# Kernel optimization log

Hardware: AMD Instinct MI355X
Metric: run time of the kernel (lower is better)

The kernel has to match this reference:

```python
import jax, jax.numpy as jnp
import numpy as np

B, H, W, D, K = 32, 64, 64, 128, 1024

def setup_inputs() -> dict:
    key = jax.random.key(0)
    k1, k2 = jax.random.split(key)
    inputs = jax.random.normal(k1, (B, H, W, D), dtype=jnp.float32)
    embedding = jax.random.normal(k2, (D, K), dtype=jnp.float32)  # codebook, column per code
    return {"inputs": inputs, "embedding": embedding}

def reference(inputs, embedding):
    D_ = embedding.shape[0]
    x = inputs.reshape(-1, D_)                                  # [N, D]
    dist = (jnp.sum(x * x, axis=-1, keepdims=True)
            - 2.0 * (x @ embedding)
            + jnp.sum(embedding * embedding, axis=0, keepdims=True))  # [N, K]
    idx = jnp.argmax(-dist, axis=1).reshape(inputs.shape[:-1])  # [B, H, W]
    return embedding.T[idx]                                     # [B, H, W, D]
```

## Files before the change

### kernel.cpp

```cpp
#include <hip/hip_runtime.h>

#define KC 1024
#define DD 128
#define NT_COUNT (KC / 16)
#define RPB 64

typedef short bf16x8 __attribute__((ext_vector_type(8)));
typedef float f32x4  __attribute__((ext_vector_type(4)));

#define AS1 __attribute__((address_space(1)))
#define AS3 __attribute__((address_space(3)))

static __device__ __forceinline__ unsigned short f2bf(float f) {
    unsigned u = __float_as_uint(f);
    unsigned r = (u + 0x7fffu + ((u >> 16) & 1u)) >> 16;
    return (unsigned short)r;
}
static __device__ __forceinline__ float bf2f(unsigned short h) {
    return __uint_as_float(((unsigned)h) << 16);
}
static __device__ __forceinline__ void gl_lds16(const void* g, void* l) {
    __builtin_amdgcn_global_load_lds((const AS1 void*)g, (AS3 void*)l, 16, 0, 0);
}
static __device__ __forceinline__ void gl_lds4(const void* g, void* l) {
    __builtin_amdgcn_global_load_lds((const AS1 void*)g, (AS3 void*)l, 4, 0, 0);
}

__global__ __launch_bounds__(256) void vq_prep(const float* __restrict__ E,
                                               float* __restrict__ e2h,
                                               float* __restrict__ ET,
                                               unsigned short* __restrict__ Bpk) {
    __shared__ float T[16 * 129];
    const int nt  = blockIdx.x;
    const int tid = threadIdx.x;

    for (int i = tid; i < 16 * DD; i += 256) {
        int d  = i >> 4;
        int kk = i & 15;
        T[kk * 129 + d] = E[(size_t)d * KC + nt * 16 + kk];
    }
    __syncthreads();

    if (tid < 16) {
        float s = 0.f;
#pragma unroll 16
        for (int d = 0; d < DD; ++d) {
            float v = T[tid * 129 + d];
            s = fmaf(v, v, s);
        }
        e2h[nt * 16 + tid] = 512.0f - 0.5f * s;
    }

    for (int i = tid; i < 16 * DD; i += 256) {
        int kk = i >> 7;
        int d  = i & 127;
        ET[(size_t)(nt * 16 + kk) * DD + d] = T[kk * 129 + d];
    }

    {
        const int s    = tid >> 6;
        const int lane = tid & 63;
        const int kk   = lane & 15;
        const int d0   = s * 32 + (lane >> 4) * 8;
        bf16x8 hi, lo;
#pragma unroll
        for (int j = 0; j < 8; ++j) {
            float v = T[kk * 129 + d0 + j];
            unsigned short h = f2bf(v);
            hi[j] = (short)h;
            lo[j] = (short)f2bf(v - bf2f(h));
        }
        char* base = (char*)Bpk + (size_t)nt * 8192 + s * 1024 + lane * 16;
        *(bf16x8*)(base)        = hi;
        *(bf16x8*)(base + 4096) = lo;
    }
}

__global__ __launch_bounds__(64, 2) void vq_main(const float* __restrict__ X,
                                                 const float* __restrict__ e2h,
                                                 const float* __restrict__ ET,
                                                 const unsigned short* __restrict__ Bpk,
                                                 float* __restrict__ Out) {
    __shared__ __align__(16) char lds[2 * 8448];
    int*   s_k1  = (int*)(lds);
    int*   s_k2  = (int*)(lds + 256);
    int*   s_win = (int*)(lds + 512);
    float* s_gap = (float*)(lds + 768);

    const int lane  = threadIdx.x;
    const int quad  = lane >> 4;
    const int n16   = lane & 15;
    const int wrow0 = blockIdx.x * RPB;
    const int lidx16 = lane * 16;
    const int lidx4  = lane * 4;

    bf16x8 ahi[4][4], alo[4][4];
#pragma unroll
    for (int t = 0; t < 4; ++t) {
#pragma unroll
        for (int s = 0; s < 4; ++s) {
            const int row = wrow0 + t * 16 + n16;
            const int d0  = s * 32 + quad * 8;
            const float4 p = *(const float4*)(X + (size_t)row * DD + d0);
            const float4 q = *(const float4*)(X + (size_t)row * DD + d0 + 4);
            float v[8] = {p.x, p.y, p.z, p.w, q.x, q.y, q.z, q.w};
#pragma unroll
            for (int j = 0; j < 8; ++j) {
                unsigned short h = f2bf(v[j]);
                ahi[t][s][j] = (short)h;
                alo[t][s][j] = (short)f2bf(v[j] - bf2f(h));
            }
        }
    }

    float p1[4][4], p2[4][4];
#pragma unroll
    for (int t = 0; t < 4; ++t)
#pragma unroll
        for (int r = 0; r < 4; ++r) { p1[t][r] = 0.0f; p2[t][r] = 0.0f; }

#define STAGE(NT, BOFF)                                                          \
    do {                                                                         \
        const char* g = (const char*)Bpk + (size_t)(NT) * 8192;                  \
        _Pragma("unroll")                                                        \
        for (int c = 0; c < 8; ++c)                                              \
            gl_lds16(g + c * 1024 + lidx16, lds + (BOFF) + c * 1024);            \
        gl_lds4(e2h + (NT) * 16 + n16, lds + (BOFF) + 8192);                     \
    } while (0)

#define TILE(NT, BOFF)                                                           \
    do {                                                                         \
        const char* l = lds + (BOFF);                                            \
        const bf16x8 bh0 = *(const bf16x8*)(l + 0 * 1024 + lidx16);              \
        const bf16x8 bh1 = *(const bf16x8*)(l + 1 * 1024 + lidx16);              \
        const bf16x8 bh2 = *(const bf16x8*)(l + 2 * 1024 + lidx16);              \
        const bf16x8 bh3 = *(const bf16x8*)(l + 3 * 1024 + lidx16);              \
        const bf16x8 bl0 = *(const bf16x8*)(l + 4 * 1024 + lidx16);              \
        const bf16x8 bl1 = *(const bf16x8*)(l + 5 * 1024 + lidx16);              \
        const bf16x8 bl2 = *(const bf16x8*)(l + 6 * 1024 + lidx16);              \
        const bf16x8 bl3 = *(const bf16x8*)(l + 7 * 1024 + lidx16);              \
        const float  ev  = *(const float*)(l + 8192 + lidx4);                    \
        const unsigned ntinv = (unsigned)(63 - (NT));                            \
        _Pragma("unroll")                                                        \
        for (int t = 0; t < 4; ++t) {                                            \
            f32x4 acc = {ev, ev, ev, ev};                                        \
            acc = __builtin_amdgcn_mfma_f32_16x16x32_bf16(ahi[t][0], bh0, acc, 0, 0, 0); \
            acc = __builtin_amdgcn_mfma_f32_16x16x32_bf16(ahi[t][1], bh1, acc, 0, 0, 0); \
            acc = __builtin_amdgcn_mfma_f32_16x16x32_bf16(ahi[t][2], bh2, acc, 0, 0, 0); \
            acc = __builtin_amdgcn_mfma_f32_16x16x32_bf16(ahi[t][3], bh3, acc, 0, 0, 0); \
            acc = __builtin_amdgcn_mfma_f32_16x16x32_bf16(alo[t][0], bh0, acc, 0, 0, 0); \
            acc = __builtin_amdgcn_mfma_f32_16x16x32_bf16(alo[t][1], bh1, acc, 0, 0, 0); \
            acc = __builtin_amdgcn_mfma_f32_16x16x32_bf16(alo[t][2], bh2, acc, 0, 0, 0); \
            acc = __builtin_amdgcn_mfma_f32_16x16x32_bf16(alo[t][3], bh3, acc, 0, 0, 0); \
            acc = __builtin_amdgcn_mfma_f32_16x16x32_bf16(ahi[t][0], bl0, acc, 0, 0, 0); \
            acc = __builtin_amdgcn_mfma_f32_16x16x32_bf16(ahi[t][1], bl1, acc, 0, 0, 0); \
            acc = __builtin_amdgcn_mfma_f32_16x16x32_bf16(ahi[t][2], bl2, acc, 0, 0, 0); \
            acc = __builtin_amdgcn_mfma_f32_16x16x32_bf16(ahi[t][3], bl3, acc, 0, 0, 0); \
            _Pragma("unroll")                                                    \
            for (int r = 0; r < 4; ++r) {                                        \
                float v = __uint_as_float((__float_as_uint(acc[r]) & ~63u) | ntinv); \
                float lo = fminf(p1[t][r], v);                                   \
                p1[t][r] = fmaxf(p1[t][r], v);                                   \
                p2[t][r] = fmaxf(p2[t][r], lo);                                  \
            }                                                                    \
        }                                                                        \
    } while (0)

    STAGE(0, 0);
    for (int nt = 0; nt < NT_COUNT; nt += 2) {
        STAGE(nt + 1, 8448);
        __builtin_amdgcn_s_waitcnt(3961);
        __builtin_amdgcn_sched_barrier(0);
        TILE(nt, 0);
        if (nt + 2 < NT_COUNT) {
            STAGE(nt + 2, 0);
            __builtin_amdgcn_s_waitcnt(3961);
        } else {
            __builtin_amdgcn_s_waitcnt(3952);
        }
        __builtin_amdgcn_sched_barrier(0);
        TILE(nt + 1, 8448);
    }
#undef STAGE
#undef TILE

#pragma unroll
    for (int t = 0; t < 4; ++t) {
#pragma unroll
        for (int r = 0; r < 4; ++r) {
            unsigned u1 = __float_as_uint(p1[t][r]);
            unsigned u2 = __float_as_uint(p2[t][r]);
            int k1 = (int)(63u - (u1 & 63u)) * 16 + n16;
            int k2 = (int)(63u - (u2 & 63u)) * 16 + n16;
            unsigned long long q1 =
                ((unsigned long long)(u1 & ~63u) << 32) | (unsigned)(1023 - k1);
            unsigned long long q2 =
                ((unsigned long long)(u2 & ~63u) << 32) | (unsigned)(1023 - k2);
#pragma unroll
            for (int m = 1; m < 16; m <<= 1) {
                unsigned long long o1 = __shfl_xor(q1, m, 64);
                unsigned long long o2 = __shfl_xor(q2, m, 64);
                unsigned long long lo = q1 < o1 ? q1 : o1;
                q1 = q1 > o1 ? q1 : o1;
                unsigned long long hi2 = q2 > o2 ? q2 : o2;
                q2 = lo > hi2 ? lo : hi2;
            }
            if (n16 == 0) {
                int row = t * 16 + quad * 4 + r;
                s_k1[row] = 1023 - (int)(q1 & 1023u);
                s_k2[row] = 1023 - (int)(q2 & 1023u);
                s_gap[row] = __uint_as_float((unsigned)(q1 >> 32)) -
                             __uint_as_float((unsigned)(q2 >> 32));
            }
        }
    }
    __syncthreads();

    {
        const int k1 = s_k1[lane];
        const int k2 = s_k2[lane];
        int win = k1;
        if (s_gap[lane] < 0.5f) {
            const float4* __restrict__ xr  = (const float4*)(X + (size_t)(wrow0 + lane) * DD);
            const float4* __restrict__ e1  = (const float4*)(ET + (size_t)k1 * DD);
            const float4* __restrict__ e2p = (const float4*)(ET + (size_t)k2 * DD);
            double dot1 = 0.0, ee1 = 0.0, dot2 = 0.0, ee2 = 0.0;
#pragma unroll 4
            for (int d4 = 0; d4 < DD / 4; ++d4) {
                const float4 xv = xr[d4];
                const float4 v1 = e1[d4];
                const float4 v2 = e2p[d4];
                const float xs[4] = {xv.x, xv.y, xv.z, xv.w};
                const float a1[4] = {v1.x, v1.y, v1.z, v1.w};
                const float a2[4] = {v2.x, v2.y, v2.z, v2.w};
#pragma unroll
                for (int j = 0; j < 4; ++j) {
                    const double xd  = (double)xs[j];
                    const double v1d = (double)a1[j];
                    const double v2d = (double)a2[j];
                    dot1 = fma(xd, v1d, dot1);
                    ee1  = fma(v1d, v1d, ee1);
                    dot2 = fma(xd, v2d, dot2);
                    ee2  = fma(v2d, v2d, ee2);
                }
            }
            double d1 = ee1 - 2.0 * dot1;
            double d2 = ee2 - 2.0 * dot2;
            win = (d2 < d1 || (d2 == d1 && k2 < k1)) ? k2 : k1;
        }
        s_win[lane] = win;
    }
    __syncthreads();

    for (int i = lane; i < RPB * (DD / 4); i += 64) {
        const int row = i >> 5;
        const int d4  = i & 31;
        const float4 v = *(const float4*)(ET + (size_t)s_win[row] * DD + d4 * 4);
        *(float4*)(Out + (size_t)(wrow0 + row) * DD + d4 * 4) = v;
    }
}

extern "C" void kernel_launch(void* const* d_in, const int* in_sizes, int n_in,
                              void* d_out, int out_size, void* d_ws, size_t ws_size,
                              hipStream_t stream) {
    const float* X = (const float*)d_in[0];
    const float* E = (const float*)d_in[1];
    float* Out = (float*)d_out;

    float* e2h = (float*)d_ws;
    float* ET  = e2h + KC;
    unsigned short* Bpk = (unsigned short*)(ET + (size_t)KC * DD);

    const int N = in_sizes[0] / DD;

    hipLaunchKernelGGL(vq_prep, dim3(NT_COUNT), dim3(256), 0, stream, E, e2h, ET, Bpk);
    hipLaunchKernelGGL(vq_main, dim3(N / RPB), dim3(64), 0, stream,
                       X, e2h, ET, Bpk, Out);
}
```

Before: 215.2 us.

## Share codebook tiles across four waves with cooperative 4-deep LDS pipeline

Changes the main kernel from a single 64-row wave per block to four waves per block covering 128 rows (32 rows each). Each codebook tile is loaded into LDS cooperatively, with each wave fetching a quarter, and staged through a 4-slot ring buffer two tiles ahead with a block barrier per tile. The codebook norms are preloaded once into LDS. This cuts redundant global/L2 traffic for the codebook and halves per-wave register use, in exchange for a block-wide barrier every tile and less MFMA work per B-fragment load.

```diff
diff --git a/kernel.cpp b/kernel.cpp
--- a/kernel.cpp
+++ b/kernel.cpp
@@ -3,7 +3,7 @@
 #define KC 1024
 #define DD 128
 #define NT_COUNT (KC / 16)
-#define RPB 64
+#define RPB 128
 
 typedef short bf16x8 __attribute__((ext_vector_type(8)));
 typedef float f32x4  __attribute__((ext_vector_type(4)));
@@ -21,9 +21,6 @@
 }
 static __device__ __forceinline__ void gl_lds16(const void* g, void* l) {
     __builtin_amdgcn_global_load_lds((const AS1 void*)g, (AS3 void*)l, 16, 0, 0);
-}
-static __device__ __forceinline__ void gl_lds4(const void* g, void* l) {
-    __builtin_amdgcn_global_load_lds((const AS1 void*)g, (AS3 void*)l, 4, 0, 0);
 }
 
 __global__ __launch_bounds__(256) void vq_prep(const float* __restrict__ E,
@@ -76,27 +73,31 @@
     }
 }
 
-__global__ __launch_bounds__(64, 2) void vq_main(const float* __restrict__ X,
-                                                 const float* __restrict__ e2h,
-                                                 const float* __restrict__ ET,
-                                                 const unsigned short* __restrict__ Bpk,
-                                                 float* __restrict__ Out) {
-    __shared__ __align__(16) char lds[2 * 8448];
+__global__ __launch_bounds__(256, 4) void vq_main(const float* __restrict__ X,
+                                                  const float* __restrict__ e2h,
+                                                  const float* __restrict__ ET,
+                                                  const unsigned short* __restrict__ Bpk,
+                                                  float* __restrict__ Out) {
+    __shared__ __align__(16) char lds[4 * 8192 + 4096];
+    float* s_e2  = (float*)(lds + 32768);
     int*   s_k1  = (int*)(lds);
-    int*   s_k2  = (int*)(lds + 256);
-    int*   s_win = (int*)(lds + 512);
-    float* s_gap = (float*)(lds + 768);
-
-    const int lane  = threadIdx.x;
-    const int quad  = lane >> 4;
-    const int n16   = lane & 15;
-    const int wrow0 = blockIdx.x * RPB;
+    int*   s_k2  = (int*)(lds + 512);
+    float* s_gap = (float*)(lds + 1024);
+    int*   s_win = (int*)(lds + 1536);
+
+    const int tid  = threadIdx.x;
+    const int lane = tid & 63;
+    const int wid  = tid >> 6;
+    const int quad = lane >> 4;
+    const int n16  = lane & 15;
+    const int wrow0 = blockIdx.x * RPB + wid * 32;
     const int lidx16 = lane * 16;
-    const int lidx4  = lane * 4;
-
-    bf16x8 ahi[4][4], alo[4][4];
-#pragma unroll
-    for (int t = 0; t < 4; ++t) {
+
+    for (int i = tid; i < KC; i += 256) s_e2[i] = e2h[i];
+
+    bf16x8 ahi[2][4], alo[2][4];
+#pragma unroll
+    for (int t = 0; t < 2; ++t) {
 #pragma unroll
         for (int s = 0; s < 4; ++s) {
             const int row = wrow0 + t * 16 + n16;
@@ -113,19 +114,20 @@
         }
     }
 
-    float p1[4][4], p2[4][4];
-#pragma unroll
-    for (int t = 0; t < 4; ++t)
+    float p1[2][4], p2[2][4];
+#pragma unroll
+    for (int t = 0; t < 2; ++t)
 #pragma unroll
         for (int r = 0; r < 4; ++r) { p1[t][r] = 0.0f; p2[t][r] = 0.0f; }
+
+    __syncthreads();
 
 #define STAGE(NT, BOFF)                                                          \
     do {                                                                         \
-        const char* g = (const char*)Bpk + (size_t)(NT) * 8192;                  \
-        _Pragma("unroll")                                                        \
-        for (int c = 0; c < 8; ++c)                                              \
-            gl_lds16(g + c * 1024 + lidx16, lds + (BOFF) + c * 1024);            \
-        gl_lds4(e2h + (NT) * 16 + n16, lds + (BOFF) + 8192);                     \
+        const char* g = (const char*)Bpk + (size_t)(NT) * 8192 + wid * 2048;     \
+        char* l = lds + (BOFF) + wid * 2048;                                     \
+        gl_lds16(g + lidx16, l);                                                 \
+        gl_lds16(g + 1024 + lidx16, l + 1024);                                   \
     } while (0)
 
 #define TILE(NT, BOFF)                                                           \
@@ -139,10 +141,10 @@
         const bf16x8 bl1 = *(const bf16x8*)(l + 5 * 1024 + lidx16);              \
         const bf16x8 bl2 = *(const bf16x8*)(l + 6 * 1024 + lidx16);              \
         const bf16x8 bl3 = *(const bf16x8*)(l + 7 * 1024 + lidx16);              \
-        const float  ev  = *(const float*)(l + 8192 + lidx4);                    \
+        const float  ev  = s_e2[(NT) * 16 + n16];                                \
         const unsigned ntinv = (unsigned)(63 - (NT));                            \
         _Pragma("unroll")                                                        \
-        for (int t = 0; t < 4; ++t) {                                            \
+        for (int t = 0; t < 2; ++t) {                                            \
             f32x4 acc = {ev, ev, ev, ev};                                        \
             acc = __builtin_amdgcn_mfma_f32_16x16x32_bf16(ahi[t][0], bh0, acc, 0, 0, 0); \
             acc = __builtin_amdgcn_mfma_f32_16x16x32_bf16(ahi[t][1], bh1, acc, 0, 0, 0); \
@@ -167,25 +169,27 @@
     } while (0)
 
     STAGE(0, 0);
-    for (int nt = 0; nt < NT_COUNT; nt += 2) {
-        STAGE(nt + 1, 8448);
-        __builtin_amdgcn_s_waitcnt(3961);
-        __builtin_amdgcn_sched_barrier(0);
-        TILE(nt, 0);
+    STAGE(1, 8192);
+    __builtin_amdgcn_sched_barrier(0);
+    for (int nt = 0; nt < NT_COUNT; ++nt) {
         if (nt + 2 < NT_COUNT) {
-            STAGE(nt + 2, 0);
-            __builtin_amdgcn_s_waitcnt(3961);
+            STAGE(nt + 2, ((nt + 2) & 3) * 8192);
+            __builtin_amdgcn_s_waitcnt(3956);
+        } else if (nt == NT_COUNT - 2) {
+            __builtin_amdgcn_s_waitcnt(3954);
         } else {
             __builtin_amdgcn_s_waitcnt(3952);
         }
         __builtin_amdgcn_sched_barrier(0);
-        TILE(nt + 1, 8448);
+        __builtin_amdgcn_s_barrier();
+        __builtin_amdgcn_sched_barrier(0);
+        TILE(nt, (nt & 3) * 8192);
     }
 #undef STAGE
 #undef TILE
 
 #pragma unroll
-    for (int t = 0; t < 4; ++t) {
+    for (int t = 0; t < 2; ++t) {
 #pragma unroll
         for (int r = 0; r < 4; ++r) {
             unsigned u1 = __float_as_uint(p1[t][r]);
@@ -206,7 +210,7 @@
                 q2 = lo > hi2 ? lo : hi2;
             }
             if (n16 == 0) {
-                int row = t * 16 + quad * 4 + r;
+                int row = wid * 32 + t * 16 + quad * 4 + r;
                 s_k1[row] = 1023 - (int)(q1 & 1023u);
                 s_k2[row] = 1023 - (int)(q2 & 1023u);
                 s_gap[row] = __uint_as_float((unsigned)(q1 >> 32)) -
@@ -216,12 +220,12 @@
     }
     __syncthreads();
 
-    {
-        const int k1 = s_k1[lane];
-        const int k2 = s_k2[lane];
+    if (tid < RPB) {
+        const int k1 = s_k1[tid];
+        const int k2 = s_k2[tid];
         int win = k1;
-        if (s_gap[lane] < 0.5f) {
-            const float4* __restrict__ xr  = (const float4*)(X + (size_t)(wrow0 + lane) * DD);
+        if (s_gap[tid] < 0.5f) {
+            const float4* __restrict__ xr  = (const float4*)(X + (size_t)(blockIdx.x * RPB + tid) * DD);
             const float4* __restrict__ e1  = (const float4*)(ET + (size_t)k1 * DD);
             const float4* __restrict__ e2p = (const float4*)(ET + (size_t)k2 * DD);
             double dot1 = 0.0, ee1 = 0.0, dot2 = 0.0, ee2 = 0.0;
@@ -248,15 +252,15 @@
             double d2 = ee2 - 2.0 * dot2;
             win = (d2 < d1 || (d2 == d1 && k2 < k1)) ? k2 : k1;
         }
-        s_win[lane] = win;
-    }
-    __syncthreads();
-
-    for (int i = lane; i < RPB * (DD / 4); i += 64) {
+        s_win[tid] = win;
+    }
+    __syncthreads();
+
+    for (int i = tid; i < RPB * (DD / 4); i += 256) {
         const int row = i >> 5;
         const int d4  = i & 31;
         const float4 v = *(const float4*)(ET + (size_t)s_win[row] * DD + d4 * 4);
-        *(float4*)(Out + (size_t)(wrow0 + row) * DD + d4 * 4) = v;
+        *(float4*)(Out + (size_t)(blockIdx.x * RPB + row) * DD + d4 * 4) = v;
     }
 }
 
@@ -274,6 +278,6 @@
     const int N = in_sizes[0] / DD;
 
     hipLaunchKernelGGL(vq_prep, dim3(NT_COUNT), dim3(256), 0, stream, E, e2h, ET, Bpk);
-    hipLaunchKernelGGL(vq_main, dim3(N / RPB), dim3(64), 0, stream,
+    hipLaunchKernelGGL(vq_main, dim3(N / RPB), dim3(256), 0, stream,
                        X, e2h, ET, Bpk, Out);
 }
```

After: 226.4 us. 1.05x slower.

## Triple-buffer codebook tiles, interleave async loads with MFMA clusters, split accumulators

Applied to the files above, without the earlier changes.

Moves from double to triple buffering of the packed codebook tiles in LDS, keeping two tiles in flight. The global-to-LDS loads for a future tile are now spread between the four per-row-tile MFMA clusters instead of issued in one burst. Each cluster accumulates into three independent accumulator chains that are summed at the end, which shortens the dependent MFMA chain. This costs more LDS per block, and the changed summation order can alter rounding and therefore argmax ties.

```diff
diff --git a/kernel.cpp b/kernel.cpp
--- a/kernel.cpp
+++ b/kernel.cpp
@@ -81,7 +81,7 @@
                                                  const float* __restrict__ ET,
                                                  const unsigned short* __restrict__ Bpk,
                                                  float* __restrict__ Out) {
-    __shared__ __align__(16) char lds[2 * 8448];
+    __shared__ __align__(16) char lds[3 * 8448];
     int*   s_k1  = (int*)(lds);
     int*   s_k2  = (int*)(lds + 256);
     int*   s_win = (int*)(lds + 512);
@@ -119,17 +119,37 @@
 #pragma unroll
         for (int r = 0; r < 4; ++r) { p1[t][r] = 0.0f; p2[t][r] = 0.0f; }
 
-#define STAGE(NT, BOFF)                                                          \
+#define CLUSTER(T)                                                               \
     do {                                                                         \
-        const char* g = (const char*)Bpk + (size_t)(NT) * 8192;                  \
+        f32x4 aA = {ev, ev, ev, ev};                                             \
+        f32x4 aB = {0.f, 0.f, 0.f, 0.f};                                         \
+        f32x4 aC = {0.f, 0.f, 0.f, 0.f};                                         \
+        aA = __builtin_amdgcn_mfma_f32_16x16x32_bf16(ahi[T][0], bh0, aA, 0, 0, 0); \
+        aB = __builtin_amdgcn_mfma_f32_16x16x32_bf16(alo[T][0], bh0, aB, 0, 0, 0); \
+        aC = __builtin_amdgcn_mfma_f32_16x16x32_bf16(ahi[T][0], bl0, aC, 0, 0, 0); \
+        aA = __builtin_amdgcn_mfma_f32_16x16x32_bf16(ahi[T][1], bh1, aA, 0, 0, 0); \
+        aB = __builtin_amdgcn_mfma_f32_16x16x32_bf16(alo[T][1], bh1, aB, 0, 0, 0); \
+        aC = __builtin_amdgcn_mfma_f32_16x16x32_bf16(ahi[T][1], bl1, aC, 0, 0, 0); \
+        aA = __builtin_amdgcn_mfma_f32_16x16x32_bf16(ahi[T][2], bh2, aA, 0, 0, 0); \
+        aB = __builtin_amdgcn_mfma_f32_16x16x32_bf16(alo[T][2], bh2, aB, 0, 0, 0); \
+        aC = __builtin_amdgcn_mfma_f32_16x16x32_bf16(ahi[T][2], bl2, aC, 0, 0, 0); \
+        aA = __builtin_amdgcn_mfma_f32_16x16x32_bf16(ahi[T][3], bh3, aA, 0, 0, 0); \
+        aB = __builtin_amdgcn_mfma_f32_16x16x32_bf16(alo[T][3], bh3, aB, 0, 0, 0); \
+        aC = __builtin_amdgcn_mfma_f32_16x16x32_bf16(ahi[T][3], bl3, aC, 0, 0, 0); \
         _Pragma("unroll")                                                        \
-        for (int c = 0; c < 8; ++c)                                              \
-            gl_lds16(g + c * 1024 + lidx16, lds + (BOFF) + c * 1024);            \
-        gl_lds4(e2h + (NT) * 16 + n16, lds + (BOFF) + 8192);                     \
+        for (int r = 0; r < 4; ++r) {                                            \
+            float sv = (aA[r] + aB[r]) + aC[r];                                  \
+            float v = __uint_as_float((__float_as_uint(sv) & ~63u) | ntinv);     \
+            float lo = fminf(p1[T][r], v);                                       \
+            p1[T][r] = fmaxf(p1[T][r], v);                                       \
+            p2[T][r] = fmaxf(p2[T][r], lo);                                      \
+        }                                                                        \
     } while (0)
 
-#define TILE(NT, BOFF)                                                           \
+#define BODY(NT, BOFF, SNT, SBOFF, DOSTAGE, WENC)                                \
     do {                                                                         \
+        __builtin_amdgcn_s_waitcnt(WENC);                                        \
+        __builtin_amdgcn_sched_barrier(0);                                       \
         const char* l = lds + (BOFF);                                            \
         const bf16x8 bh0 = *(const bf16x8*)(l + 0 * 1024 + lidx16);              \
         const bf16x8 bh1 = *(const bf16x8*)(l + 1 * 1024 + lidx16);              \
@@ -141,48 +161,58 @@
         const bf16x8 bl3 = *(const bf16x8*)(l + 7 * 1024 + lidx16);              \
         const float  ev  = *(const float*)(l + 8192 + lidx4);                    \
         const unsigned ntinv = (unsigned)(63 - (NT));                            \
+        const char* g = (const char*)Bpk + (size_t)(SNT) * 8192;                 \
+        char* sl = lds + (SBOFF);                                                \
+        if (DOSTAGE) {                                                           \
+            gl_lds16(g + 0 * 1024 + lidx16, sl + 0 * 1024);                      \
+            gl_lds16(g + 1 * 1024 + lidx16, sl + 1 * 1024);                      \
+            gl_lds16(g + 2 * 1024 + lidx16, sl + 2 * 1024);                      \
+        }                                                                        \
+        __builtin_amdgcn_sched_barrier(0);                                       \
+        CLUSTER(0);                                                              \
+        if (DOSTAGE) {                                                           \
+            gl_lds16(g + 3 * 1024 + lidx16, sl + 3 * 1024);                      \
+            gl_lds16(g + 4 * 1024 + lidx16, sl + 4 * 1024);                      \
+        }                                                                        \
+        __builtin_amdgcn_sched_barrier(0);                                       \
+        CLUSTER(1);                                                              \
+        if (DOSTAGE) {                                                           \
+            gl_lds16(g + 5 * 1024 + lidx16, sl + 5 * 1024);                      \
+            gl_lds16(g + 6 * 1024 + lidx16, sl + 6 * 1024);                      \
+        }                                                                        \
+        __builtin_amdgcn_sched_barrier(0);                                       \
+        CLUSTER(2);                                                              \
+        if (DOSTAGE) {                                                           \
+            gl_lds16(g + 7 * 1024 + lidx16, sl + 7 * 1024);                      \
+            gl_lds4(e2h + (SNT) * 16 + n16, sl + 8192);                          \
+        }                                                                        \
+        __builtin_amdgcn_sched_barrier(0);                                       \
+        CLUSTER(3);                                                              \
+    } while (0)
+
+#define STAGE_ALL(NT, BOFF)                                                      \
+    do {                                                                         \
+        const char* g = (const char*)Bpk + (size_t)(NT) * 8192;                  \
         _Pragma("unroll")                                                        \
-        for (int t = 0; t < 4; ++t) {                                            \
-            f32x4 acc = {ev, ev, ev, ev};                                        \
-            acc = __builtin_amdgcn_mfma_f32_16x16x32_bf16(ahi[t][0], bh0, acc, 0, 0, 0); \
-            acc = __builtin_amdgcn_mfma_f32_16x16x32_bf16(ahi[t][1], bh1, acc, 0, 0, 0); \
-            acc = __builtin_amdgcn_mfma_f32_16x16x32_bf16(ahi[t][2], bh2, acc, 0, 0, 0); \
-            acc = __builtin_amdgcn_mfma_f32_16x16x32_bf16(ahi[t][3], bh3, acc, 0, 0, 0); \
-            acc = __builtin_amdgcn_mfma_f32_16x16x32_bf16(alo[t][0], bh0, acc, 0, 0, 0); \
-            acc = __builtin_amdgcn_mfma_f32_16x16x32_bf16(alo[t][1], bh1, acc, 0, 0, 0); \
-            acc = __builtin_amdgcn_mfma_f32_16x16x32_bf16(alo[t][2], bh2, acc, 0, 0, 0); \
-            acc = __builtin_amdgcn_mfma_f32_16x16x32_bf16(alo[t][3], bh3, acc, 0, 0, 0); \
-            acc = __builtin_amdgcn_mfma_f32_16x16x32_bf16(ahi[t][0], bl0, acc, 0, 0, 0); \
-            acc = __builtin_amdgcn_mfma_f32_16x16x32_bf16(ahi[t][1], bl1, acc, 0, 0, 0); \
-            acc = __builtin_amdgcn_mfma_f32_16x16x32_bf16(ahi[t][2], bl2, acc, 0, 0, 0); \
-            acc = __builtin_amdgcn_mfma_f32_16x16x32_bf16(ahi[t][3], bl3, acc, 0, 0, 0); \
-            _Pragma("unroll")                                                    \
-            for (int r = 0; r < 4; ++r) {                                        \
-                float v = __uint_as_float((__float_as_uint(acc[r]) & ~63u) | ntinv); \
-                float lo = fminf(p1[t][r], v);                                   \
-                p1[t][r] = fmaxf(p1[t][r], v);                                   \
-                p2[t][r] = fmaxf(p2[t][r], lo);                                  \
-            }                                                                    \
-        }                                                                        \
+        for (int c = 0; c < 8; ++c)                                              \
+            gl_lds16(g + c * 1024 + lidx16, lds + (BOFF) + c * 1024);            \
+        gl_lds4(e2h + (NT) * 16 + n16, lds + (BOFF) + 8192);                     \
     } while (0)
 
-    STAGE(0, 0);
-    for (int nt = 0; nt < NT_COUNT; nt += 2) {
-        STAGE(nt + 1, 8448);
-        __builtin_amdgcn_s_waitcnt(3961);
-        __builtin_amdgcn_sched_barrier(0);
-        TILE(nt, 0);
-        if (nt + 2 < NT_COUNT) {
-            STAGE(nt + 2, 0);
-            __builtin_amdgcn_s_waitcnt(3961);
-        } else {
-            __builtin_amdgcn_s_waitcnt(3952);
-        }
-        __builtin_amdgcn_sched_barrier(0);
-        TILE(nt + 1, 8448);
-    }
-#undef STAGE
-#undef TILE
+    STAGE_ALL(0, 0);
+    STAGE_ALL(1, 8448);
+    for (int nt = 0; nt < NT_COUNT - 4; nt += 3) {
+        BODY(nt,     0,        nt + 2, 16896, 1, 3961);
+        BODY(nt + 1, 8448,     nt + 3, 0,     1, 3961);
+        BODY(nt + 2, 16896,    nt + 4, 8448,  1, 3961);
+    }
+    BODY(60, 0,     62, 16896, 1, 3961);
+    BODY(61, 8448,  63, 0,     1, 3961);
+    BODY(62, 16896, 0,  0,     0, 3961);
+    BODY(63, 0,     0,  0,     0, 3952);
+#undef BODY
+#undef CLUSTER
+#undef STAGE_ALL
 
 #pragma unroll
     for (int t = 0; t < 4; ++t) {
```

Measured after the change: 292.8 us. +36.1%, slower.

## Switch distance GEMM to 32x32x16 MFMA tiles with 32-code codebook blocks

Applied to the files above, without the earlier changes.

Replaces the 16x16x32 bf16 MFMA tiling with 32x32x16 MFMA: each wave now holds two 32-row A tiles and processes 32 codes per tile, staged in two halves. The codebook packing in the prep kernel changes to match. The code-norm bias now comes from a per-block LDS copy of all norms rather than being streamed alongside each tile. This is meant to cut B-fragment LDS reads per FLOP and issue fewer, larger MFMAs. In exchange it raises register pressure (two 16-wide accumulators plus 32 running max/second-max values) and lowers the index-tag bits from 6 to 5, which adds a wider 32-lane shuffle reduction.

```diff
diff --git a/kernel.cpp b/kernel.cpp
--- a/kernel.cpp
+++ b/kernel.cpp
@@ -2,14 +2,17 @@
 
 #define KC 1024
 #define DD 128
-#define NT_COUNT (KC / 16)
+#define NT32 32
 #define RPB 64
 
-typedef short bf16x8 __attribute__((ext_vector_type(8)));
-typedef float f32x4  __attribute__((ext_vector_type(4)));
+typedef short bf16x8  __attribute__((ext_vector_type(8)));
+typedef float f32x16  __attribute__((ext_vector_type(16)));
 
 #define AS1 __attribute__((address_space(1)))
 #define AS3 __attribute__((address_space(3)))
+
+#define VMC8 3960
+#define VMC0 3952
 
 static __device__ __forceinline__ unsigned short f2bf(float f) {
     unsigned u = __float_as_uint(f);
@@ -22,57 +25,55 @@
 static __device__ __forceinline__ void gl_lds16(const void* g, void* l) {
     __builtin_amdgcn_global_load_lds((const AS1 void*)g, (AS3 void*)l, 16, 0, 0);
 }
-static __device__ __forceinline__ void gl_lds4(const void* g, void* l) {
-    __builtin_amdgcn_global_load_lds((const AS1 void*)g, (AS3 void*)l, 4, 0, 0);
-}
 
 __global__ __launch_bounds__(256) void vq_prep(const float* __restrict__ E,
                                                float* __restrict__ e2h,
                                                float* __restrict__ ET,
                                                unsigned short* __restrict__ Bpk) {
-    __shared__ float T[16 * 129];
+    __shared__ float T[32 * 129];
     const int nt  = blockIdx.x;
     const int tid = threadIdx.x;
 
-    for (int i = tid; i < 16 * DD; i += 256) {
-        int d  = i >> 4;
-        int kk = i & 15;
-        T[kk * 129 + d] = E[(size_t)d * KC + nt * 16 + kk];
-    }
-    __syncthreads();
-
-    if (tid < 16) {
+    for (int i = tid; i < 32 * DD; i += 256) {
+        int d  = i >> 5;
+        int kk = i & 31;
+        T[kk * 129 + d] = E[(size_t)d * KC + nt * 32 + kk];
+    }
+    __syncthreads();
+
+    if (tid < 32) {
         float s = 0.f;
 #pragma unroll 16
         for (int d = 0; d < DD; ++d) {
             float v = T[tid * 129 + d];
             s = fmaf(v, v, s);
         }
-        e2h[nt * 16 + tid] = 512.0f - 0.5f * s;
-    }
-
-    for (int i = tid; i < 16 * DD; i += 256) {
+        e2h[nt * 32 + tid] = 512.0f - 0.5f * s;
+    }
+
+    for (int i = tid; i < 32 * DD; i += 256) {
         int kk = i >> 7;
         int d  = i & 127;
-        ET[(size_t)(nt * 16 + kk) * DD + d] = T[kk * 129 + d];
-    }
-
-    {
-        const int s    = tid >> 6;
+        ET[(size_t)(nt * 32 + kk) * DD + d] = T[kk * 129 + d];
+    }
+
+#pragma unroll
+    for (int it = 0; it < 2; ++it) {
+        const int s    = (tid >> 6) + 4 * it;
         const int lane = tid & 63;
-        const int kk   = lane & 15;
-        const int d0   = s * 32 + (lane >> 4) * 8;
+        const int code = lane & 31;
+        const int kb   = s * 16 + (lane >> 5) * 8;
         bf16x8 hi, lo;
 #pragma unroll
         for (int j = 0; j < 8; ++j) {
-            float v = T[kk * 129 + d0 + j];
+            float v = T[code * 129 + kb + j];
             unsigned short h = f2bf(v);
             hi[j] = (short)h;
             lo[j] = (short)f2bf(v - bf2f(h));
         }
-        char* base = (char*)Bpk + (size_t)nt * 8192 + s * 1024 + lane * 16;
+        char* base = (char*)Bpk + (size_t)nt * 16384 + (s >> 2) * 8192 + (s & 3) * 2048 + lane * 16;
         *(bf16x8*)(base)        = hi;
-        *(bf16x8*)(base + 4096) = lo;
+        *(bf16x8*)(base + 1024) = lo;
     }
 }
 
@@ -81,132 +82,134 @@
                                                  const float* __restrict__ ET,
                                                  const unsigned short* __restrict__ Bpk,
                                                  float* __restrict__ Out) {
-    __shared__ __align__(16) char lds[2 * 8448];
+    __shared__ __align__(16) char lds[2 * 8192];
+    __shared__ float s_e2[KC];
     int*   s_k1  = (int*)(lds);
     int*   s_k2  = (int*)(lds + 256);
     int*   s_win = (int*)(lds + 512);
     float* s_gap = (float*)(lds + 768);
 
     const int lane  = threadIdx.x;
-    const int quad  = lane >> 4;
-    const int n16   = lane & 15;
+    const int l31   = lane & 31;
+    const int khalf = lane >> 5;
     const int wrow0 = blockIdx.x * RPB;
     const int lidx16 = lane * 16;
-    const int lidx4  = lane * 4;
-
-    bf16x8 ahi[4][4], alo[4][4];
-#pragma unroll
-    for (int t = 0; t < 4; ++t) {
-#pragma unroll
-        for (int s = 0; s < 4; ++s) {
-            const int row = wrow0 + t * 16 + n16;
-            const int d0  = s * 32 + quad * 8;
+
+    bf16x8 ahi[2][8], alo[2][8];
+#pragma unroll
+    for (int m = 0; m < 2; ++m) {
+#pragma unroll
+        for (int s = 0; s < 8; ++s) {
+            const int row = wrow0 + m * 32 + l31;
+            const int d0  = s * 16 + khalf * 8;
             const float4 p = *(const float4*)(X + (size_t)row * DD + d0);
             const float4 q = *(const float4*)(X + (size_t)row * DD + d0 + 4);
             float v[8] = {p.x, p.y, p.z, p.w, q.x, q.y, q.z, q.w};
 #pragma unroll
             for (int j = 0; j < 8; ++j) {
                 unsigned short h = f2bf(v[j]);
-                ahi[t][s][j] = (short)h;
-                alo[t][s][j] = (short)f2bf(v[j] - bf2f(h));
-            }
-        }
-    }
-
-    float p1[4][4], p2[4][4];
-#pragma unroll
-    for (int t = 0; t < 4; ++t)
-#pragma unroll
-        for (int r = 0; r < 4; ++r) { p1[t][r] = 0.0f; p2[t][r] = 0.0f; }
-
-#define STAGE(NT, BOFF)                                                          \
+                ahi[m][s][j] = (short)h;
+                alo[m][s][j] = (short)f2bf(v[j] - bf2f(h));
+            }
+        }
+    }
+
+    for (int i = lane; i < KC; i += 64) s_e2[i] = e2h[i];
+    __syncthreads();
+
+    float p1[2][16], p2[2][16];
+#pragma unroll
+    for (int m = 0; m < 2; ++m)
+#pragma unroll
+        for (int r = 0; r < 16; ++r) { p1[m][r] = 0.0f; p2[m][r] = 0.0f; }
+
+#define STAGE(H, BOFF)                                                           \
     do {                                                                         \
-        const char* g = (const char*)Bpk + (size_t)(NT) * 8192;                  \
+        const char* g = (const char*)Bpk + (size_t)(H) * 8192;                   \
         _Pragma("unroll")                                                        \
         for (int c = 0; c < 8; ++c)                                              \
             gl_lds16(g + c * 1024 + lidx16, lds + (BOFF) + c * 1024);            \
-        gl_lds4(e2h + (NT) * 16 + n16, lds + (BOFF) + 8192);                     \
     } while (0)
 
-#define TILE(NT, BOFF)                                                           \
+#define MM(acc, af, bf) acc = __builtin_amdgcn_mfma_f32_32x32x16_bf16(af, bf, acc, 0, 0, 0)
+
+#define HALF(BOFF, HF)                                                           \
     do {                                                                         \
         const char* l = lds + (BOFF);                                            \
-        const bf16x8 bh0 = *(const bf16x8*)(l + 0 * 1024 + lidx16);              \
-        const bf16x8 bh1 = *(const bf16x8*)(l + 1 * 1024 + lidx16);              \
-        const bf16x8 bh2 = *(const bf16x8*)(l + 2 * 1024 + lidx16);              \
-        const bf16x8 bh3 = *(const bf16x8*)(l + 3 * 1024 + lidx16);              \
-        const bf16x8 bl0 = *(const bf16x8*)(l + 4 * 1024 + lidx16);              \
-        const bf16x8 bl1 = *(const bf16x8*)(l + 5 * 1024 + lidx16);              \
-        const bf16x8 bl2 = *(const bf16x8*)(l + 6 * 1024 + lidx16);              \
-        const bf16x8 bl3 = *(const bf16x8*)(l + 7 * 1024 + lidx16);              \
-        const float  ev  = *(const float*)(l + 8192 + lidx4);                    \
-        const unsigned ntinv = (unsigned)(63 - (NT));                            \
         _Pragma("unroll")                                                        \
-        for (int t = 0; t < 4; ++t) {                                            \
-            f32x4 acc = {ev, ev, ev, ev};                                        \
-            acc = __builtin_amdgcn_mfma_f32_16x16x32_bf16(ahi[t][0], bh0, acc, 0, 0, 0); \
-            acc = __builtin_amdgcn_mfma_f32_16x16x32_bf16(ahi[t][1], bh1, acc, 0, 0, 0); \
-            acc = __builtin_amdgcn_mfma_f32_16x16x32_bf16(ahi[t][2], bh2, acc, 0, 0, 0); \
-            acc = __builtin_amdgcn_mfma_f32_16x16x32_bf16(ahi[t][3], bh3, acc, 0, 0, 0); \
-            acc = __builtin_amdgcn_mfma_f32_16x16x32_bf16(alo[t][0], bh0, acc, 0, 0, 0); \
-            acc = __builtin_amdgcn_mfma_f32_16x16x32_bf16(alo[t][1], bh1, acc, 0, 0, 0); \
-            acc = __builtin_amdgcn_mfma_f32_16x16x32_bf16(alo[t][2], bh2, acc, 0, 0, 0); \
-            acc = __builtin_amdgcn_mfma_f32_16x16x32_bf16(alo[t][3], bh3, acc, 0, 0, 0); \
-            acc = __builtin_amdgcn_mfma_f32_16x16x32_bf16(ahi[t][0], bl0, acc, 0, 0, 0); \
-            acc = __builtin_amdgcn_mfma_f32_16x16x32_bf16(ahi[t][1], bl1, acc, 0, 0, 0); \
-            acc = __builtin_amdgcn_mfma_f32_16x16x32_bf16(ahi[t][2], bl2, acc, 0, 0, 0); \
-            acc = __builtin_amdgcn_mfma_f32_16x16x32_bf16(ahi[t][3], bl3, acc, 0, 0, 0); \
-            _Pragma("unroll")                                                    \
-            for (int r = 0; r < 4; ++r) {                                        \
-                float v = __uint_as_float((__float_as_uint(acc[r]) & ~63u) | ntinv); \
-                float lo = fminf(p1[t][r], v);                                   \
-                p1[t][r] = fmaxf(p1[t][r], v);                                   \
-                p2[t][r] = fmaxf(p2[t][r], lo);                                  \
-            }                                                                    \
+        for (int sl = 0; sl < 4; ++sl) {                                         \
+            const bf16x8 bh = *(const bf16x8*)(l + sl * 2048 + lidx16);          \
+            const bf16x8 bl = *(const bf16x8*)(l + sl * 2048 + 1024 + lidx16);   \
+            const int sg = (HF) * 4 + sl;                                        \
+            MM(accA, ahi[0][sg], bh);                                            \
+            MM(accB, ahi[1][sg], bh);                                            \
+            MM(accA, alo[0][sg], bh);                                            \
+            MM(accB, alo[1][sg], bh);                                            \
+            MM(accA, ahi[0][sg], bl);                                            \
+            MM(accB, ahi[1][sg], bl);                                            \
         }                                                                        \
     } while (0)
 
     STAGE(0, 0);
-    for (int nt = 0; nt < NT_COUNT; nt += 2) {
-        STAGE(nt + 1, 8448);
-        __builtin_amdgcn_s_waitcnt(3961);
+    for (int h = 0; h < 64; h += 2) {
+        const int nt = h >> 1;
+        const float ev = s_e2[nt * 32 + l31];
+        f32x16 accA, accB;
+#pragma unroll
+        for (int r = 0; r < 16; ++r) { accA[r] = ev; accB[r] = ev; }
+
+        STAGE(h + 1, 8192);
+        __builtin_amdgcn_s_waitcnt(VMC8);
         __builtin_amdgcn_sched_barrier(0);
-        TILE(nt, 0);
-        if (nt + 2 < NT_COUNT) {
-            STAGE(nt + 2, 0);
-            __builtin_amdgcn_s_waitcnt(3961);
+        HALF(0, 0);
+        if (h + 2 < 64) {
+            STAGE(h + 2, 0);
+            __builtin_amdgcn_s_waitcnt(VMC8);
         } else {
-            __builtin_amdgcn_s_waitcnt(3952);
+            __builtin_amdgcn_s_waitcnt(VMC0);
         }
         __builtin_amdgcn_sched_barrier(0);
-        TILE(nt + 1, 8448);
-    }
+        HALF(8192, 1);
+
+        const unsigned ntinv = (unsigned)(31 - nt);
+#pragma unroll
+        for (int m = 0; m < 2; ++m)
+#pragma unroll
+            for (int r = 0; r < 16; ++r) {
+                float sv = (m == 0) ? accA[r] : accB[r];
+                float v = __uint_as_float((__float_as_uint(sv) & ~31u) | ntinv);
+                float lo = fminf(p1[m][r], v);
+                p1[m][r] = fmaxf(p1[m][r], v);
+                p2[m][r] = fmaxf(p2[m][r], lo);
+            }
+    }
+#undef HALF
+#undef MM
 #undef STAGE
-#undef TILE
-
-#pragma unroll
-    for (int t = 0; t < 4; ++t) {
-#pragma unroll
-        for (int r = 0; r < 4; ++r) {
-            unsigned u1 = __float_as_uint(p1[t][r]);
-            unsigned u2 = __float_as_uint(p2[t][r]);
-            int k1 = (int)(63u - (u1 & 63u)) * 16 + n16;
-            int k2 = (int)(63u - (u2 & 63u)) * 16 + n16;
+
+#pragma unroll
+    for (int m = 0; m < 2; ++m) {
+#pragma unroll
+        for (int r = 0; r < 16; ++r) {
+            unsigned u1 = __float_as_uint(p1[m][r]);
+            unsigned u2 = __float_as_uint(p2[m][r]);
+            int k1 = (int)(31u - (u1 & 31u)) * 32 + l31;
+            int k2 = (int)(31u - (u2 & 31u)) * 32 + l31;
             unsigned long long q1 =
-                ((unsigned long long)(u1 & ~63u) << 32) | (unsigned)(1023 - k1);
+                ((unsigned long long)(u1 & ~31u) << 32) | (unsigned)(1023 - k1);
             unsigned long long q2 =
-                ((unsigned long long)(u2 & ~63u) << 32) | (unsigned)(1023 - k2);
-#pragma unroll
-            for (int m = 1; m < 16; m <<= 1) {
-                unsigned long long o1 = __shfl_xor(q1, m, 64);
-                unsigned long long o2 = __shfl_xor(q2, m, 64);
+                ((unsigned long long)(u2 & ~31u) << 32) | (unsigned)(1023 - k2);
+#pragma unroll
+            for (int mm = 1; mm < 32; mm <<= 1) {
+                unsigned long long o1 = __shfl_xor(q1, mm, 64);
+                unsigned long long o2 = __shfl_xor(q2, mm, 64);
                 unsigned long long lo = q1 < o1 ? q1 : o1;
                 q1 = q1 > o1 ? q1 : o1;
                 unsigned long long hi2 = q2 > o2 ? q2 : o2;
                 q2 = lo > hi2 ? lo : hi2;
             }
-            if (n16 == 0) {
-                int row = t * 16 + quad * 4 + r;
+            if (l31 == 0) {
+                int row = m * 32 + (r & 3) + 8 * (r >> 2) + 4 * khalf;
                 s_k1[row] = 1023 - (int)(q1 & 1023u);
                 s_k2[row] = 1023 - (int)(q2 & 1023u);
                 s_gap[row] = __uint_as_float((unsigned)(q1 >> 32)) -
@@ -273,7 +276,7 @@
 
     const int N = in_sizes[0] / DD;
 
-    hipLaunchKernelGGL(vq_prep, dim3(NT_COUNT), dim3(256), 0, stream, E, e2h, ET, Bpk);
+    hipLaunchKernelGGL(vq_prep, dim3(NT32), dim3(256), 0, stream, E, e2h, ET, Bpk);
     hipLaunchKernelGGL(vq_main, dim3(N / RPB), dim3(64), 0, stream,
                        X, e2h, ET, Bpk, Out);
 }
```

New measurement: 242.5 us. 12.7% more time.
